# Kernel optimization log

Measured on AMD Instinct MI355X. Metric: run time of the kernel, lower is better.

## Reference

```python
import jax, jax.numpy as jnp
import numpy as np

K = 4          # temporal_depth
IN_SIZE = 1024 # conv input channels
DN = ('NCDHW', 'OIDHW', 'NCDHW')


def setup_inputs() -> dict:
    key = jax.random.key(0)
    ks = jax.random.split(key, 12)
    B, T, C, H, W = 1, 8, IN_SIZE, 14, 14
    s = 0.02
    return {
        'videos': jax.random.normal(ks[0], (B, T, C, H, W), dtype=jnp.float32),
        # Conv3d(in_size, in_size, 3, padding='same')
        'conv1_w': jax.random.normal(ks[1], (IN_SIZE, IN_SIZE, 3, 3, 3), dtype=jnp.float32) * s,
        'conv1_b': jax.random.normal(ks[2], (IN_SIZE,), dtype=jnp.float32) * s,
        # Conv3d(in_size, 512, 3, padding='same')
        'conv2_w': jax.random.normal(ks[3], (512, IN_SIZE, 3, 3, 3), dtype=jnp.float32) * s,
        'conv2_b': jax.random.normal(ks[4], (512,), dtype=jnp.float32) * s,
        # Linear(512,512) -> Linear(512,512) -> Linear(512,128), torch (out,in) layout
        'l1_w': jax.random.normal(ks[5], (512, 512), dtype=jnp.float32) * s,
        'l1_b': jax.random.normal(ks[6], (512,), dtype=jnp.float32) * s,
        'l2_w': jax.random.normal(ks[7], (512, 512), dtype=jnp.float32) * s,
        'l2_b': jax.random.normal(ks[8], (512,), dtype=jnp.float32) * s,
        'l3_w': jax.random.normal(ks[9], (128, 512), dtype=jnp.float32) * s,
        'l3_b': jax.random.normal(ks[10], (128,), dtype=jnp.float32) * s,
    }


def reference(videos, conv1_w, conv1_b, conv2_w, conv2_b,
              l1_w, l1_b, l2_w, l2_b, l3_w, l3_b):
    B, T, C, H, W = videos.shape
    # prepend k zero frames, as in the torch code
    padded = jnp.concatenate(
        [jnp.zeros((B, K, C, H, W), videos.dtype), videos], axis=1)
    # window o covers padded frames [o, o+K) -> strictly-past original frames
    idx = jnp.arange(T)[:, None] + jnp.arange(K)[None, :]      # (T, K)
    win = padded[:, idx]                                        # (B, T, K, C, H, W)
    # permute(1,0,2,3): channels first, depth=K -> batch all windows together
    win = win.transpose(0, 1, 3, 2, 4, 5).reshape(B * T, C, K, H, W)
    # Conv3d + ReLU + Conv3d + ReLU, each with 'same' zero padding per window
    h = jax.lax.conv_general_dilated(win, conv1_w, (1, 1, 1), 'SAME',
                                     dimension_numbers=DN)
    h = jax.nn.relu(h + conv1_b[None, :, None, None, None])
    h = jax.lax.conv_general_dilated(h, conv2_w, (1, 1, 1), 'SAME',
                                     dimension_numbers=DN)
    h = jax.nn.relu(h + conv2_b[None, :, None, None, None])
    # MaxPool3d over the full (D,H,W) extent == global max per channel
    pooled = jnp.max(h, axis=(2, 3, 4))                         # (B*T, 512)
    x = jax.nn.relu(pooled @ l1_w.T + l1_b)
    x = jax.nn.relu(x @ l2_w.T + l2_b)
    x = jax.nn.relu(x @ l3_w.T + l3_b)                          # (B*T, 128)
    return x.reshape(B, T, 128)
```

## Files before the change

### kernel.cpp

```cpp
#include <hip/hip_runtime.h>

typedef __attribute__((ext_vector_type(8))) short short8;
typedef __attribute__((ext_vector_type(4))) int int4v;
typedef __attribute__((ext_vector_type(4))) float floatx4;
typedef __attribute__((ext_vector_type(4))) unsigned short ushort4v;

#define DEV __device__ __forceinline__

constexpr int M_TOT = 6272;
constexpr int M_PAD = 6400;

DEV void async_ld16(const void* g, void* l) {
  __builtin_amdgcn_global_load_lds(
      (const __attribute__((address_space(1))) unsigned int*)g,
      (__attribute__((address_space(3))) unsigned int*)l,
      16, 0, 0);
}

DEV unsigned short f2bf(float x) {
  union { float f; unsigned int u; } v; v.f = x;
  unsigned int u = v.u;
  u += 0x7FFFu + ((u >> 16) & 1u);
  return (unsigned short)(u >> 16);
}

DEV float bf2f(unsigned short s) {
  union { unsigned int u; float f; } v; v.u = ((unsigned int)s) << 16;
  return v.f;
}

__global__ void wtrans(const float* __restrict__ w, unsigned short* __restrict__ wt,
                       int total ) {
  __shared__ unsigned short l[256 * 27];
  const int tid  = threadIdx.x;
  const int base = blockIdx.x * 256;
  #pragma unroll 1
  for (int j = tid; j < 256 * 27; j += 256)
    l[j] = f2bf(w[(size_t)base * 27 + j]);
  __syncthreads();
  #pragma unroll 1
  for (int tap = 0; tap < 27; ++tap)
    wt[(size_t)tap * total + base + tid] = l[tid * 27 + tap];
}

__global__ void build_P1(const float* __restrict__ videos, unsigned short* __restrict__ P1) {
  const int f  = blockIdx.x;
  const int c0 = blockIdx.y * 64;
  const int tid = threadIdx.x;
  __shared__ unsigned short tile[64][196];

  #pragma unroll 1
  for (int it = 0; it < 49; ++it) {
    int idx = it * 256 + tid;
    int c = idx / 196, r = idx - c * 196;
    tile[c][r] = f2bf(videos[(size_t)(f * 1024 + c0 + c) * 196 + r]);
  }
  __syncthreads();

  const int c   = tid & 63;
  const int hwq = tid >> 6;
  #pragma unroll 1
  for (int s = 1; s <= 4; ++s) {
    int t = f + 5 - s;
    if (t > 7) continue;
    unsigned short* dst = P1 + (size_t)(t * 6 + s) * 256 * 1024 + (size_t)c0;
    #pragma unroll 1
    for (int it = 0; it < 49; ++it) {
      int hw = it * 4 + hwq;
      int h = hw / 14, w = hw - h * 14;
      dst[(size_t)((h + 1) * 16 + (w + 1)) * 1024 + c] = tile[c][hw];
    }
  }
}

#define DSR(dst, addr, off) \
  asm volatile("ds_read_b128 %0, %1 offset:" #off : "=&v"(dst) : "v"(addr))
#define WAITL(n) \
  asm volatile("s_waitcnt lgkmcnt(" #n ")" ::: "memory"); \
  __builtin_amdgcn_sched_barrier(0)

template <int COUT, bool TCOND>
__global__ __launch_bounds__(512, 2) void conv_gemm(
    const unsigned short* __restrict__ P,
    const unsigned short* __restrict__ Wt,
    const unsigned int* __restrict__ sched,
    unsigned short* __restrict__ part)
{
  constexpr int CIN = 1024;
  __shared__ short lA[4][8192];
  __shared__ short lB[4][8192];
  const int tid  = threadIdx.x;
  const int wave = tid >> 6;
  const int lane = tid & 63;

  const unsigned int e = sched[blockIdx.x];
  const int x2   = e & 31;
  const int nidx = (e >> 5) & 3;
  const int zs   = (e >> 7) & 7;
  const int tap0 = (e >> 10) & 31;
  const int tap1 = (e >> 15) & 31;
  const int m0 = x2 * 256;
  const int n0 = nidx * 256;
  unsigned short* partOut = part + (size_t)zs * M_PAD * COUT;

  bool kdv[3] = {false, false, false};
  {
    const int cA = m0 / 196;
    int cB = (m0 + 255) / 196; if (cB > 31) cB = 31;
    for (int c = cA; c <= cB; ++c) {
      int t = c >> 2, d = c & 3;
      #pragma unroll
      for (int kd = 0; kd < 3; ++kd) {
        int s = d + kd;
        bool ok = (s >= 1) && (s <= 4);
        if (TCOND) ok = ok && (s >= 5 - t);
        kdv[kd] = kdv[kd] || ok;
      }
    }
  }

  const int arow = tid >> 2;
  const int aswz = (((tid & 3) ^ ((arow >> 1) & 3)) << 4);
  int aG[2], bG[2];
  #pragma unroll
  for (int q = 0; q < 2; ++q) {
    int m = m0 + q * 128 + arow;
    int t = m / 784;  int r2 = m - t * 784;
    int d = r2 / 196; int r3 = r2 - d * 196;
    int h = r3 / 14;  int w = r3 - h * 14;
    aG[q] = ((((t * 6 + d) * 16 + h) * 16 + w) * CIN) * 2 + aswz;
    bG[q] = (n0 + q * 128 + arow) * (CIN * 2) + aswz;
  }

  int nvt = 0;
  for (int tp = tap0; tp < tap1; ++tp) if (kdv[tp / 9]) ++nvt;
  const int steps = nvt * 32;
  int tap_s = tap0;
  while (tap_s < tap1 && !kdv[tap_s / 9]) ++tap_s;
  int c_s = 0;
  int stA = 0, stB = 0;
  auto setBases = [&]() {
    const int kd = tap_s / 9, rm = tap_s - kd * 9;
    const int kh = rm / 3, kw = rm - kh * 3;
    stA = ((((kd * 16) + kh) * 16 + kw) * CIN) * 2 + c_s * 2;
    stB = tap_s * (COUT * CIN * 2) + c_s * 2;
  };
  auto adv = [&]() {
    c_s += 32;
    if (c_s == CIN) { c_s = 0; do { ++tap_s; } while (tap_s < tap1 && !kdv[tap_s / 9]); }
  };

  const char* Pb = (const char*)P;
  const char* Wb = (const char*)Wt;
  char* lAc = (char*)&lA[0][0];
  char* lBc = (char*)&lB[0][0];
  const unsigned ldsA0 =
      (unsigned)(size_t)(__attribute__((address_space(3))) char*)lAc;
  const unsigned ldsB0 =
      (unsigned)(size_t)(__attribute__((address_space(3))) char*)lBc;

  const int nst = steps < 3 ? steps : 3;
  #pragma unroll 1
  for (int s = 0; s < nst; ++s) {
    setBases();
    char* dA = lAc + s * 16384;
    char* dB = lBc + s * 16384;
    async_ld16(Pb + aG[0] + stA, dA + tid * 16);
    async_ld16(Wb + bG[0] + stB, dB + tid * 16);
    async_ld16(Pb + aG[1] + stA, dA + 8192 + tid * 16);
    async_ld16(Wb + bG[1] + stB, dB + 8192 + tid * 16);
    adv();
  }
  if (nst >= 3)      asm volatile("s_waitcnt vmcnt(8)" ::: "memory");
  else if (nst == 2) asm volatile("s_waitcnt vmcnt(4)" ::: "memory");
  else               asm volatile("s_waitcnt vmcnt(0)" ::: "memory");
  __builtin_amdgcn_s_barrier();
  __builtin_amdgcn_sched_barrier(0);

  const int wm   = (wave >> 2) * 128;
  const int wn   = (wave & 3) * 64;
  const int quad = lane >> 4;
  const int l15  = lane & 15;
  const int segc = ((quad ^ ((l15 >> 1) & 3)) << 4);
  const unsigned rowA = ((unsigned)(wm + l15) << 6) + segc;
  const unsigned rowB = ((unsigned)(wn + l15) << 6) + segc;

  floatx4 acc[8][4];
  const floatx4 zero4 = {0.f, 0.f, 0.f, 0.f};
  #pragma unroll
  for (int i = 0; i < 8; ++i)
    #pragma unroll
    for (int j = 0; j < 4; ++j) acc[i][j] = zero4;

  #pragma unroll 1
  for (int t = 0; t < steps; ++t) {
    const unsigned slot = (unsigned)(t & 3) * 16384u;
    const unsigned aBase = ldsA0 + slot + rowA;
    const unsigned bBase = ldsB0 + slot + rowB;
    const bool h3s = (t + 3 < steps);
    const bool h2s = (t + 2 < steps);
    char* dA = lAc + ((t + 3) & 3) * 16384;
    char* dB = lBc + ((t + 3) & 3) * 16384;
    if (h3s) setBases();

    int4v bv[4], av[8];
    DSR(bv[0], bBase, 0);
    DSR(bv[1], bBase, 1024);
    DSR(bv[2], bBase, 2048);
    DSR(bv[3], bBase, 3072);
    DSR(av[0], aBase, 0);
    DSR(av[1], aBase, 1024);
    DSR(av[2], aBase, 2048);
    DSR(av[3], aBase, 3072);
    DSR(av[4], aBase, 4096);
    DSR(av[5], aBase, 5120);
    DSR(av[6], aBase, 6144);
    DSR(av[7], aBase, 7168);

    if (h3s) {
      async_ld16(Pb + aG[0] + stA, dA + tid * 16);
      async_ld16(Wb + bG[0] + stB, dB + tid * 16);
      async_ld16(Pb + aG[1] + stA, dA + 8192 + tid * 16);
      async_ld16(Wb + bG[1] + stB, dB + 8192 + tid * 16);
      adv();
    }

    __builtin_amdgcn_s_setprio(1);
    short8 bs[4];
    WAITL(7);
    #pragma unroll
    for (int j = 0; j < 4; ++j) bs[j] = __builtin_bit_cast(short8, bv[j]);
    {
      short8 a = __builtin_bit_cast(short8, av[0]);
      #pragma unroll
      for (int j = 0; j < 4; ++j)
        acc[0][j] = __builtin_amdgcn_mfma_f32_16x16x32_bf16(a, bs[j], acc[0][j], 0, 0, 0);
    }
    WAITL(6);
    {
      short8 a = __builtin_bit_cast(short8, av[1]);
      #pragma unroll
      for (int j = 0; j < 4; ++j)
        acc[1][j] = __builtin_amdgcn_mfma_f32_16x16x32_bf16(a, bs[j], acc[1][j], 0, 0, 0);
    }
    WAITL(5);
    {
      short8 a = __builtin_bit_cast(short8, av[2]);
      #pragma unroll
      for (int j = 0; j < 4; ++j)
        acc[2][j] = __builtin_amdgcn_mfma_f32_16x16x32_bf16(a, bs[j], acc[2][j], 0, 0, 0);
    }
    WAITL(4);
    {
      short8 a = __builtin_bit_cast(short8, av[3]);
      #pragma unroll
      for (int j = 0; j < 4; ++j)
        acc[3][j] = __builtin_amdgcn_mfma_f32_16x16x32_bf16(a, bs[j], acc[3][j], 0, 0, 0);
    }
    WAITL(3);
    {
      short8 a = __builtin_bit_cast(short8, av[4]);
      #pragma unroll
      for (int j = 0; j < 4; ++j)
        acc[4][j] = __builtin_amdgcn_mfma_f32_16x16x32_bf16(a, bs[j], acc[4][j], 0, 0, 0);
    }
    WAITL(2);
    {
      short8 a = __builtin_bit_cast(short8, av[5]);
      #pragma unroll
      for (int j = 0; j < 4; ++j)
        acc[5][j] = __builtin_amdgcn_mfma_f32_16x16x32_bf16(a, bs[j], acc[5][j], 0, 0, 0);
    }
    WAITL(1);
    {
      short8 a = __builtin_bit_cast(short8, av[6]);
      #pragma unroll
      for (int j = 0; j < 4; ++j)
        acc[6][j] = __builtin_amdgcn_mfma_f32_16x16x32_bf16(a, bs[j], acc[6][j], 0, 0, 0);
    }
    WAITL(0);
    {
      short8 a = __builtin_bit_cast(short8, av[7]);
      #pragma unroll
      for (int j = 0; j < 4; ++j)
        acc[7][j] = __builtin_amdgcn_mfma_f32_16x16x32_bf16(a, bs[j], acc[7][j], 0, 0, 0);
    }
    __builtin_amdgcn_s_setprio(0);

    if (h3s)                asm volatile("s_waitcnt vmcnt(8)" ::: "memory");
    else if (h2s)           asm volatile("s_waitcnt vmcnt(4)" ::: "memory");
    else if (t + 1 < steps) asm volatile("s_waitcnt vmcnt(0)" ::: "memory");
    __builtin_amdgcn_sched_barrier(0);
    __builtin_amdgcn_s_barrier();
    __builtin_amdgcn_sched_barrier(0);
  }

  asm volatile("s_waitcnt vmcnt(0) lgkmcnt(0)" ::: "memory");
  __builtin_amdgcn_s_barrier();

  #pragma unroll
  for (int j = 0; j < 4; ++j) {
    const int o = n0 + wn + j * 16 + l15;
    #pragma unroll
    for (int i = 0; i < 8; ++i) {
      #pragma unroll
      for (int r = 0; r < 4; ++r) {
        int m = m0 + wm + i * 16 + quad * 4 + r;
        partOut[(size_t)m * COUT + o] = f2bf(acc[i][j][r]);
      }
    }
  }
}

__global__ void reduce_conv1(const unsigned short* __restrict__ part,
                             const float* __restrict__ bias,
                             unsigned short* __restrict__ P2) {
  const int idx = blockIdx.x * 256 + threadIdx.x;
  const int m  = idx >> 8;
  const int o4 = (idx & 255) * 4;
  const size_t ss = (size_t)M_PAD * 1024;
  const size_t base = (size_t)m * 1024 + o4;
  ushort4v p0 = *(const ushort4v*)(part + base);
  ushort4v p1 = *(const ushort4v*)(part + ss + base);
  ushort4v p2 = *(const ushort4v*)(part + 2 * ss + base);
  ushort4v out;
  #pragma unroll
  for (int k = 0; k < 4; ++k) {
    float v = bf2f(p0[k]) + bf2f(p1[k]) + bf2f(p2[k]) + bias[o4 + k];
    out[k] = f2bf(v > 0.f ? v : 0.f);
  }
  int t = m / 784;  int r2 = m - t * 784;
  int d = r2 / 196; int r3 = r2 - d * 196;
  int h = r3 / 14;  int w = r3 - h * 14;
  size_t didx = (size_t)(((t * 6 + d + 1) * 16 + (h + 1)) * 16 + (w + 1)) * 1024 + o4;
  *(ushort4v*)(P2 + didx) = out;
}

__global__ void reduce_conv2(const unsigned short* __restrict__ part,
                             const float* __restrict__ bias,
                             unsigned short* __restrict__ h2) {
  const int idx = blockIdx.x * 256 + threadIdx.x;
  const int m  = idx >> 7;
  const int o4 = (idx & 127) * 4;
  const size_t base = (size_t)m * 512 + o4;
  const size_t ss = (size_t)M_PAD * 512;
  float acc[4];
  #pragma unroll
  for (int k = 0; k < 4; ++k) acc[k] = bias[o4 + k];
  #pragma unroll
  for (int s = 0; s < 5; ++s) {
    ushort4v p = *(const ushort4v*)(part + (size_t)s * ss + base);
    #pragma unroll
    for (int k = 0; k < 4; ++k) acc[k] += bf2f(p[k]);
  }
  ushort4v out;
  #pragma unroll
  for (int k = 0; k < 4; ++k) out[k] = f2bf(acc[k] > 0.f ? acc[k] : 0.f);
  *(ushort4v*)(h2 + base) = out;
}

__global__ void pool1(const unsigned short* __restrict__ h2,
                      unsigned short* __restrict__ partial) {
  const int t = blockIdx.x / 28, ch = blockIdx.x % 28, o = threadIdx.x;
  const unsigned short* src = h2 + ((size_t)t * 784 + ch * 28) * 512 + o;
  unsigned short m = 0;
  #pragma unroll 4
  for (int i = 0; i < 28; ++i) { unsigned short v = src[(size_t)i * 512]; m = v > m ? v : m; }
  partial[((size_t)t * 28 + ch) * 512 + o] = m;
}

__global__ void pool2(const unsigned short* __restrict__ partial, float* __restrict__ pooled) {
  const int t = blockIdx.x, o = threadIdx.x;
  const unsigned short* src = partial + (size_t)t * 28 * 512 + o;
  unsigned short m = 0;
  #pragma unroll 4
  for (int i = 0; i < 28; ++i) { unsigned short v = src[(size_t)i * 512]; m = v > m ? v : m; }
  pooled[t * 512 + o] = bf2f(m);
}

__global__ void mlp_kernel(const float* __restrict__ pooled,
                           const float* __restrict__ w1, const float* __restrict__ b1,
                           const float* __restrict__ w2, const float* __restrict__ b2,
                           const float* __restrict__ w3, const float* __restrict__ b3,
                           float* __restrict__ out) {
  const int t = blockIdx.x, j = threadIdx.x;
  __shared__ float xa[512], xb[512];
  xa[j] = pooled[t * 512 + j];
  __syncthreads();
  {
    const float4* wr = (const float4*)(w1 + (size_t)j * 512);
    float s = b1[j];
    #pragma unroll 4
    for (int k = 0; k < 128; ++k) {
      float4 wv = wr[k];
      s += wv.x * xa[4*k] + wv.y * xa[4*k+1] + wv.z * xa[4*k+2] + wv.w * xa[4*k+3];
    }
    xb[j] = fmaxf(s, 0.f);
  }
  __syncthreads();
  {
    const float4* wr = (const float4*)(w2 + (size_t)j * 512);
    float s = b2[j];
    #pragma unroll 4
    for (int k = 0; k < 128; ++k) {
      float4 wv = wr[k];
      s += wv.x * xb[4*k] + wv.y * xb[4*k+1] + wv.z * xb[4*k+2] + wv.w * xb[4*k+3];
    }
    xa[j] = fmaxf(s, 0.f);
  }
  __syncthreads();
  if (j < 128) {
    const float4* wr = (const float4*)(w3 + (size_t)j * 512);
    float s = b3[j];
    #pragma unroll 4
    for (int k = 0; k < 128; ++k) {
      float4 wv = wr[k];
      s += wv.x * xa[4*k] + wv.y * xa[4*k+1] + wv.z * xa[4*k+2] + wv.w * xa[4*k+3];
    }
    out[t * 128 + j] = fmaxf(s, 0.f);
  }
}

static int build_sched(bool conv1, unsigned int* out) {
  const int nt = conv1 ? 4 : 2;
  unsigned int L[256];
  int cnt = 0;
  for (int n = 0; n < nt; ++n) {
    for (int x2 = 0; x2 < 25; ++x2) {
      const int m0 = x2 * 256;
      bool kdv[3] = {false, false, false};
      const int cA = m0 / 196;
      int cB = (m0 + 255) / 196; if (cB > 31) cB = 31;
      for (int c = cA; c <= cB; ++c) {
        int t = c >> 2, d = c & 3;
        for (int kd = 0; kd < 3; ++kd) {
          int s = d + kd;
          bool ok = (s >= 1 && s <= 4);
          if (conv1) ok = ok && (s >= 5 - t);
          kdv[kd] = kdv[kd] || ok;
        }
      }
      int vt[27], nv = 0;
      for (int tp = 0; tp < 27; ++tp) if (kdv[tp / 9]) vt[nv++] = tp;
      if (!nv) continue;
      const int ns = conv1 ? (nv / 9) : ((nv == 27) ? 5 : 4);
      for (int s = 0; s < ns; ++s) {
        int b0 = nv * s / ns, b1 = nv * (s + 1) / ns;
        int tp0 = vt[b0], tp1 = vt[b1 - 1] + 1;
        L[cnt++] = (unsigned int)(x2 | (n << 5) | (s << 7) | (tp0 << 10) | (tp1 << 15));
      }
    }
  }
  const int q = cnt / 8, r = cnt % 8;
  int pos = 0;
  for (int b = 0; b < 8; ++b) {
    const int nb = q + (b < r ? 1 : 0);
    for (int j = 0; j < nb; ++j) out[j * 8 + b] = L[pos++];
  }
  return cnt;
}

extern "C" void kernel_launch(void* const* d_in, const int* in_sizes, int n_in,
                              void* d_out, int out_size, void* d_ws, size_t ws_size,
                              hipStream_t stream) {
  const float* videos = (const float*)d_in[0];
  const float* c1w = (const float*)d_in[1];
  const float* c1b = (const float*)d_in[2];
  const float* c2w = (const float*)d_in[3];
  const float* c2b = (const float*)d_in[4];
  const float* l1w = (const float*)d_in[5];
  const float* l1b = (const float*)d_in[6];
  const float* l2w = (const float*)d_in[7];
  const float* l2b = (const float*)d_in[8];
  const float* l3w = (const float*)d_in[9];
  const float* l3b = (const float*)d_in[10];

  char* ws = (char*)d_ws;
  unsigned short* P12   = (unsigned short*)(ws);
  unsigned short* W1t   = (unsigned short*)(ws + 26738688);
  unsigned short* W2t   = (unsigned short*)(ws + 26738688);
  unsigned short* h2    = (unsigned short*)(ws + 55050240);
  float*          pooled= (float*)(ws + 61472768);
  unsigned short* ppart = (unsigned short*)(ws + 61489152);
  unsigned short* part  = (unsigned short*)(ws + 83361792);
  unsigned int* dsched1 = (unsigned int*)(ws + 122683392);
  unsigned int* dsched2 = (unsigned int*)(ws + 122684416);
  float* out = (float*)d_out;

  static unsigned int s1h[256], s2h[256];
  const int n1 = build_sched(true,  s1h);
  const int n2 = build_sched(false, s2h);
  hipMemcpyAsync(dsched1, s1h, sizeof(s1h), hipMemcpyHostToDevice, stream);
  hipMemcpyAsync(dsched2, s2h, sizeof(s2h), hipMemcpyHostToDevice, stream);

  hipMemsetAsync(ws, 0, 26738688, stream);
  hipMemsetAsync(part, 0, 39321600, stream);

  wtrans<<<4096, 256, 0, stream>>>(c1w, W1t, 1024 * 1024);
  build_P1<<<dim3(8, 16), 256, 0, stream>>>(videos, P12);

  conv_gemm<1024, true ><<<n1, 512, 0, stream>>>(P12, W1t, dsched1, part);

  wtrans<<<2048, 256, 0, stream>>>(c2w, W2t, 512 * 1024);
  reduce_conv1<<<6272, 256, 0, stream>>>(part, c1b, P12);
  hipMemsetAsync((char*)part + 32505856, 0, 262144, stream);

  conv_gemm<512, false><<<n2, 512, 0, stream>>>(P12, W2t, dsched2, part);
  reduce_conv2<<<3136, 256, 0, stream>>>(part, c2b, h2);

  pool1<<<224, 512, 0, stream>>>(h2, ppart);
  pool2<<<8, 512, 0, stream>>>(ppart, pooled);
  mlp_kernel<<<8, 512, 0, stream>>>(pooled, l1w, l1b, l2w, l2b, l3w, l3b, out);
}
```

Baseline: 755.5 us.

## Load GEMM B operand straight from global into registers, bypassing LDS

Weight (B) fragments are now fetched by each wave with global_load_dwordx4 directly into registers, one k-step ahead, instead of being staged through a 4-deep LDS ring. The activation (A) tile stays on the async LDS pipeline with its own step counter, and the vmcnt waits are retuned for the split streams. This halves LDS usage and removes the B ds_reads. In exchange, waves sharing a column block load the same B data redundantly from L2, and B latency is hidden by only one step of prefetch. The prologue also no longer guards against fewer than three steps.

```diff
diff --git a/kernel.cpp b/kernel.cpp
--- a/kernel.cpp
+++ b/kernel.cpp
@@ -75,9 +75,12 @@
 
 #define DSR(dst, addr, off) \
   asm volatile("ds_read_b128 %0, %1 offset:" #off : "=&v"(dst) : "v"(addr))
+#define GLB(dst, p) \
+  asm volatile("global_load_dwordx4 %0, %1, off" : "=&v"(dst) : "v"(p))
 #define WAITL(n) \
   asm volatile("s_waitcnt lgkmcnt(" #n ")" ::: "memory"); \
   __builtin_amdgcn_sched_barrier(0)
+#define SB0 __builtin_amdgcn_sched_barrier(0)
 
 template <int COUT, bool TCOND>
 __global__ __launch_bounds__(512, 2) void conv_gemm(
@@ -88,7 +91,6 @@
 {
   constexpr int CIN = 1024;
   __shared__ short lA[4][8192];
-  __shared__ short lB[4][8192];
   const int tid  = threadIdx.x;
   const int wave = tid >> 6;
   const int lane = tid & 63;
@@ -121,7 +123,7 @@
 
   const int arow = tid >> 2;
   const int aswz = (((tid & 3) ^ ((arow >> 1) & 3)) << 4);
-  int aG[2], bG[2];
+  int aG[2];
   #pragma unroll
   for (int q = 0; q < 2; ++q) {
     int m = m0 + q * 128 + arow;
@@ -129,53 +131,35 @@
     int d = r2 / 196; int r3 = r2 - d * 196;
     int h = r3 / 14;  int w = r3 - h * 14;
     aG[q] = ((((t * 6 + d) * 16 + h) * 16 + w) * CIN) * 2 + aswz;
-    bG[q] = (n0 + q * 128 + arow) * (CIN * 2) + aswz;
   }
 
   int nvt = 0;
   for (int tp = tap0; tp < tap1; ++tp) if (kdv[tp / 9]) ++nvt;
   const int steps = nvt * 32;
-  int tap_s = tap0;
-  while (tap_s < tap1 && !kdv[tap_s / 9]) ++tap_s;
-  int c_s = 0;
-  int stA = 0, stB = 0;
-  auto setBases = [&]() {
-    const int kd = tap_s / 9, rm = tap_s - kd * 9;
+  int tapA = tap0;
+  while (tapA < tap1 && !kdv[tapA / 9]) ++tapA;
+  int cA2 = 0;
+  int tapB = tapA, cB2 = 0;
+  auto stepA = [&]() -> int {
+    const int kd = tapA / 9, rm = tapA - kd * 9;
     const int kh = rm / 3, kw = rm - kh * 3;
-    stA = ((((kd * 16) + kh) * 16 + kw) * CIN) * 2 + c_s * 2;
-    stB = tap_s * (COUT * CIN * 2) + c_s * 2;
+    const int st = ((((kd * 16) + kh) * 16 + kw) * CIN) * 2 + cA2 * 2;
+    cA2 += 32;
+    if (cA2 == CIN) { cA2 = 0; do { ++tapA; } while (tapA < tap1 && !kdv[tapA / 9]); }
+    return st;
   };
-  auto adv = [&]() {
-    c_s += 32;
-    if (c_s == CIN) { c_s = 0; do { ++tap_s; } while (tap_s < tap1 && !kdv[tap_s / 9]); }
+  auto stepB = [&]() -> int {
+    const int st = tapB * (COUT * CIN * 2) + cB2 * 2;
+    cB2 += 32;
+    if (cB2 == CIN) { cB2 = 0; do { ++tapB; } while (tapB < tap1 && !kdv[tapB / 9]); }
+    return st;
   };
 
   const char* Pb = (const char*)P;
   const char* Wb = (const char*)Wt;
   char* lAc = (char*)&lA[0][0];
-  char* lBc = (char*)&lB[0][0];
   const unsigned ldsA0 =
       (unsigned)(size_t)(__attribute__((address_space(3))) char*)lAc;
-  const unsigned ldsB0 =
-      (unsigned)(size_t)(__attribute__((address_space(3))) char*)lBc;
-
-  const int nst = steps < 3 ? steps : 3;
-  #pragma unroll 1
-  for (int s = 0; s < nst; ++s) {
-    setBases();
-    char* dA = lAc + s * 16384;
-    char* dB = lBc + s * 16384;
-    async_ld16(Pb + aG[0] + stA, dA + tid * 16);
-    async_ld16(Wb + bG[0] + stB, dB + tid * 16);
-    async_ld16(Pb + aG[1] + stA, dA + 8192 + tid * 16);
-    async_ld16(Wb + bG[1] + stB, dB + 8192 + tid * 16);
-    adv();
-  }
-  if (nst >= 3)      asm volatile("s_waitcnt vmcnt(8)" ::: "memory");
-  else if (nst == 2) asm volatile("s_waitcnt vmcnt(4)" ::: "memory");
-  else               asm volatile("s_waitcnt vmcnt(0)" ::: "memory");
-  __builtin_amdgcn_s_barrier();
-  __builtin_amdgcn_sched_barrier(0);
 
   const int wm   = (wave >> 2) * 128;
   const int wn   = (wave & 3) * 64;
@@ -183,7 +167,29 @@
   const int l15  = lane & 15;
   const int segc = ((quad ^ ((l15 >> 1) & 3)) << 4);
   const unsigned rowA = ((unsigned)(wm + l15) << 6) + segc;
-  const unsigned rowB = ((unsigned)(wn + l15) << 6) + segc;
+  const size_t bRowOff = ((size_t)(n0 + wn + l15) * CIN + (size_t)quad * 8) * 2;
+
+  int4v b0, b1, b2, b3;
+
+  #pragma unroll 1
+  for (int s = 0; s < 3; ++s) {
+    const int st = stepA();
+    char* dA = lAc + s * 16384;
+    async_ld16(Pb + aG[0] + st, dA + tid * 16);
+    async_ld16(Pb + aG[1] + st, dA + 8192 + tid * 16);
+  }
+  SB0;
+  {
+    const char* bp = Wb + (size_t)stepB() + bRowOff;
+    GLB(b0, bp);
+    GLB(b1, bp + 32768);
+    GLB(b2, bp + 65536);
+    GLB(b3, bp + 98304);
+  }
+  SB0;
+  asm volatile("s_waitcnt vmcnt(8)" ::: "memory");
+  __builtin_amdgcn_s_barrier();
+  SB0;
 
   floatx4 acc[8][4];
   const floatx4 zero4 = {0.f, 0.f, 0.f, 0.f};
@@ -194,20 +200,11 @@
 
   #pragma unroll 1
   for (int t = 0; t < steps; ++t) {
-    const unsigned slot = (unsigned)(t & 3) * 16384u;
-    const unsigned aBase = ldsA0 + slot + rowA;
-    const unsigned bBase = ldsB0 + slot + rowB;
+    const unsigned aBase = ldsA0 + (unsigned)(t & 3) * 16384u + rowA;
     const bool h3s = (t + 3 < steps);
-    const bool h2s = (t + 2 < steps);
-    char* dA = lAc + ((t + 3) & 3) * 16384;
-    char* dB = lBc + ((t + 3) & 3) * 16384;
-    if (h3s) setBases();
-
-    int4v bv[4], av[8];
-    DSR(bv[0], bBase, 0);
-    DSR(bv[1], bBase, 1024);
-    DSR(bv[2], bBase, 2048);
-    DSR(bv[3], bBase, 3072);
+    const bool hB  = (t + 1 < steps);
+
+    int4v av[8];
     DSR(av[0], aBase, 0);
     DSR(av[1], aBase, 1024);
     DSR(av[2], aBase, 2048);
@@ -216,20 +213,28 @@
     DSR(av[5], aBase, 5120);
     DSR(av[6], aBase, 6144);
     DSR(av[7], aBase, 7168);
+    SB0;
 
     if (h3s) {
-      async_ld16(Pb + aG[0] + stA, dA + tid * 16);
-      async_ld16(Wb + bG[0] + stB, dB + tid * 16);
-      async_ld16(Pb + aG[1] + stA, dA + 8192 + tid * 16);
-      async_ld16(Wb + bG[1] + stB, dB + 8192 + tid * 16);
-      adv();
-    }
+      const int st = stepA();
+      char* dA = lAc + ((t + 3) & 3) * 16384;
+      async_ld16(Pb + aG[0] + st, dA + tid * 16);
+      async_ld16(Pb + aG[1] + st, dA + 8192 + tid * 16);
+    }
+    SB0;
+
+    if (h3s) { asm volatile("s_waitcnt vmcnt(2)" ::: "memory"); }
+    else     { asm volatile("s_waitcnt vmcnt(0)" ::: "memory"); }
+    SB0;
+
+    short8 bs[4];
+    bs[0] = __builtin_bit_cast(short8, b0);
+    bs[1] = __builtin_bit_cast(short8, b1);
+    bs[2] = __builtin_bit_cast(short8, b2);
+    bs[3] = __builtin_bit_cast(short8, b3);
 
     __builtin_amdgcn_s_setprio(1);
-    short8 bs[4];
     WAITL(7);
-    #pragma unroll
-    for (int j = 0; j < 4; ++j) bs[j] = __builtin_bit_cast(short8, bv[j]);
     {
       short8 a = __builtin_bit_cast(short8, av[0]);
       #pragma unroll
@@ -286,13 +291,23 @@
         acc[7][j] = __builtin_amdgcn_mfma_f32_16x16x32_bf16(a, bs[j], acc[7][j], 0, 0, 0);
     }
     __builtin_amdgcn_s_setprio(0);
-
-    if (h3s)                asm volatile("s_waitcnt vmcnt(8)" ::: "memory");
-    else if (h2s)           asm volatile("s_waitcnt vmcnt(4)" ::: "memory");
-    else if (t + 1 < steps) asm volatile("s_waitcnt vmcnt(0)" ::: "memory");
-    __builtin_amdgcn_sched_barrier(0);
+    SB0;
+
+    if (hB) {
+      const char* bp = Wb + (size_t)stepB() + bRowOff;
+      GLB(b0, bp);
+      GLB(b1, bp + 32768);
+      GLB(b2, bp + 65536);
+      GLB(b3, bp + 98304);
+    }
+    SB0;
+
+    if (h3s)      { asm volatile("s_waitcnt vmcnt(6)" ::: "memory"); }
+    else if (hB)  { asm volatile("s_waitcnt vmcnt(4)" ::: "memory"); }
+    else          { asm volatile("s_waitcnt vmcnt(0)" ::: "memory"); }
+    SB0;
     __builtin_amdgcn_s_barrier();
-    __builtin_amdgcn_sched_barrier(0);
+    SB0;
   }
 
   asm volatile("s_waitcnt vmcnt(0) lgkmcnt(0)" ::: "memory");
```

Result: slower. 922.3 us (+22.1%).
